# Performance work log

Measured on AMD Instinct MI355X. Metric: run time of the kernel, lower is better.

## Reference

```python
import jax, jax.numpy as jnp
import numpy as np
import math

B, C_IN, H, W_DIM, D_DIM = 2, 128, 24, 24, 24
D_MODEL, N_HEAD, N_LAYERS, D_FF = 256, 8, 4, 512
D_K = D_MODEL // N_HEAD
EPS = 1e-6


def setup_inputs() -> dict:
    key = jax.random.key(0)
    ks = jax.random.split(key, 16)
    s = 0.02
    inp = {
        "x": jax.random.normal(ks[0], (B, C_IN, H, W_DIM, D_DIM), jnp.float32),
        # 1x1x1 Conv3d W_x: weight [out, in], bias [out]
        "Wx_w": jax.random.normal(ks[1], (D_MODEL, C_IN), jnp.float32) * s,
        "Wx_b": jnp.zeros((D_MODEL,), jnp.float32),
        # per-layer attention projections (stacked over layers)
        "Wq": jax.random.normal(ks[2], (N_LAYERS, D_MODEL, D_MODEL), jnp.float32) * s,
        "bq": jnp.zeros((N_LAYERS, D_MODEL), jnp.float32),
        "Wk": jax.random.normal(ks[3], (N_LAYERS, D_MODEL, D_MODEL), jnp.float32) * s,
        "bk": jnp.zeros((N_LAYERS, D_MODEL), jnp.float32),
        "Wv": jax.random.normal(ks[4], (N_LAYERS, D_MODEL, D_MODEL), jnp.float32) * s,
        "bv": jnp.zeros((N_LAYERS, D_MODEL), jnp.float32),
        "Wo": jax.random.normal(ks[5], (N_LAYERS, D_MODEL, D_MODEL), jnp.float32) * s,
        "bo": jnp.zeros((N_LAYERS, D_MODEL), jnp.float32),
        # layer norms
        "ln1_g": jnp.ones((N_LAYERS, D_MODEL), jnp.float32),
        "ln1_b": jnp.zeros((N_LAYERS, D_MODEL), jnp.float32),
        "ln2_g": jnp.ones((N_LAYERS, D_MODEL), jnp.float32),
        "ln2_b": jnp.zeros((N_LAYERS, D_MODEL), jnp.float32),
        # FFN
        "ffn_w1": jax.random.normal(ks[6], (N_LAYERS, D_MODEL, D_FF), jnp.float32) * s,
        "ffn_b1": jnp.zeros((N_LAYERS, D_FF), jnp.float32),
        "ffn_w2": jax.random.normal(ks[7], (N_LAYERS, D_FF, D_MODEL), jnp.float32) * s,
        "ffn_b2": jnp.zeros((N_LAYERS, D_MODEL), jnp.float32),
        # depthwise 3x3x3 conv positional encoder (groups = D_MODEL)
        "pos_w": jax.random.normal(ks[8], (N_LAYERS, D_MODEL, 1, 3, 3, 3), jnp.float32) * s,
        "pos_b": jnp.zeros((N_LAYERS, D_MODEL), jnp.float32),
    }
    return inp


def _layer_norm(t, g, b):
    mu = jnp.mean(t, axis=-1, keepdims=True)
    var = jnp.var(t, axis=-1, keepdims=True)
    return (t - mu) * jax.lax.rsqrt(var + EPS) * g + b


def reference(x, Wx_w, Wx_b, Wq, bq, Wk, bk, Wv, bv, Wo, bo,
              ln1_g, ln1_b, ln2_g, ln2_b,
              ffn_w1, ffn_b1, ffn_w2, ffn_b2, pos_w, pos_b):
    b = x.shape[0]
    # 1x1x1 conv projection W_x + ReLU (is_up=False path)
    x = jnp.einsum('bchwd,oc->bohwd', x, Wx_w) + Wx_b[None, :, None, None, None]
    x = jax.nn.relu(x)

    inv_sqrt_dk = 1.0 / math.sqrt(D_K)

    for i in range(N_LAYERS):
        # flatten spatial -> tokens: [b, n, d_model]
        t = jnp.transpose(x.reshape(b, D_MODEL, -1), (0, 2, 1))
        n = t.shape[1]

        def heads(y):  # [b,n,d] -> [b,h,n,dk]
            return jnp.transpose(y.reshape(b, n, N_HEAD, D_K), (0, 2, 1, 3))

        q = heads(t @ Wq[i] + bq[i])
        k = heads(t @ Wk[i] + bk[i])
        v = heads(t @ Wv[i] + bv[i])

        # linear attention: softmax over feature dim for q, token dim for k
        q = jax.nn.softmax(q, axis=-1) * inv_sqrt_dk
        k = jax.nn.softmax(k, axis=-2)
        ctx = jnp.einsum('bhnd,bhne->bhde', k, v)     # [b,h,dk,dk]
        o = jnp.einsum('bhnd,bhde->bhne', q, ctx)      # [b,h,n,dk]
        o = jnp.transpose(o, (0, 2, 1, 3)).reshape(b, n, D_MODEL)
        o = o @ Wo[i] + bo[i]

        t = _layer_norm(t + o, ln1_g[i], ln1_b[i])
        f = jax.nn.gelu(t @ ffn_w1[i] + ffn_b1[i], approximate=False) @ ffn_w2[i] + ffn_b2[i]
        t = _layer_norm(t + f, ln2_g[i], ln2_b[i])

        # back to volume and depthwise conv positional embedding
        x = jnp.transpose(t, (0, 2, 1)).reshape(b, D_MODEL, H, W_DIM, D_DIM)
        pos = jax.lax.conv_general_dilated(
            x, pos_w[i], window_strides=(1, 1, 1), padding='SAME',
            dimension_numbers=('NCDHW', 'OIDHW', 'NCDHW'),
            feature_group_count=D_MODEL,
        ) + pos_b[i][None, :, None, None, None]
        x = x + pos
    return x
```

## Files before the change

kernel.cpp:

```cpp
#include <hip/hip_runtime.h>
#include <math.h>

#define NTOK 13824
#define MTOT 27648
#define BATCH 2
#define CIN 128
#define DMODEL 256
#define NHEAD 8
#define NLAYERS 4
#define DFF 512
#define NSPLIT 27
#define KVHALF ((size_t)BATCH * 256 * NTOK)

typedef float f32x4 __attribute__((ext_vector_type(4)));
typedef __bf16 bf16x8 __attribute__((ext_vector_type(8)));
typedef __attribute__((address_space(1))) void gvoid;
typedef __attribute__((address_space(3))) void lvoid;

#define GLDS16(g, l) __builtin_amdgcn_global_load_lds((gvoid*)(g), (lvoid*)(l), 16, 0, 0)

__device__ __forceinline__ unsigned short f2bf(float f) {
    unsigned u = __float_as_uint(f);
    return (unsigned short)((u + 0x7FFFu + ((u >> 16) & 1u)) >> 16);
}
__device__ __forceinline__ float bf2f(unsigned short h) {
    return __uint_as_float(((unsigned)h) << 16);
}

template<int ACT, int OUTM>
__global__ __launch_bounds__(256) void gemm_bf16(
    const unsigned short* __restrict__ A, int lda,
    const unsigned short* __restrict__ Bt, int ldb,
    const float* __restrict__ bias,
    float* __restrict__ Cf, unsigned short* __restrict__ Cb,
    int ldc, int K, long sA, long sB, long sC)
{
    A  += (size_t)blockIdx.z * sA;
    Bt += (size_t)blockIdx.z * sB;
    if (OUTM == 2) Cf += (size_t)blockIdx.z * sC;
    Cb += (size_t)blockIdx.z * sC;

    int bx, by;
    {
        const int nx  = gridDim.x;
        const int q   = (nx * gridDim.y) >> 3;
        const int lin = blockIdx.y * nx + blockIdx.x;
        const int wg  = (lin & 7) * q + (lin >> 3);
        bx = wg % nx;
        by = wg / nx;
    }

    __shared__ __attribute__((aligned(16))) unsigned short As[2][8192];
    __shared__ __attribute__((aligned(16))) unsigned short Bs[2][8192];
    const int t    = threadIdx.x;
    const int lane = t & 63;
    const int wave = t >> 6;
    const int wm = wave & 1, wn = wave >> 1;
    const int m0 = bx * 128, n0 = by * 128;

    const int srow = t >> 3;
    const int skid = ((t & 7) * 8) ^ ((srow & 7) << 3);
    const unsigned short* ga = A  + (size_t)(m0 + srow) * lda + skid;
    const unsigned short* gb = Bt + (size_t)(n0 + srow) * ldb + skid;

    f32x4 acc[4][4];
    #pragma unroll
    for (int i = 0; i < 4; ++i)
        #pragma unroll
        for (int j = 0; j < 4; ++j) acc[i][j] = (f32x4)0.0f;

    const int fm  = lane & 15;
    const int fq8 = (lane >> 4) * 8;
    const int sw3 = (fm & 7) << 3;
    const int arow = (wm * 64 + fm) * 64;
    const int brow = (wn * 64 + fm) * 64;

#define STAGE(bufi, kk)                                                        \
    {                                                                          \
        _Pragma("unroll")                                                      \
        for (int p = 0; p < 4; ++p) {                                          \
            GLDS16(ga + (size_t)p * 32 * lda + (kk), &As[bufi][p * 2048 + t * 8]); \
            GLDS16(gb + (size_t)p * 32 * ldb + (kk), &Bs[bufi][p * 2048 + t * 8]); \
        }                                                                      \
    }

#define COMPUTE(bufi)                                                          \
    {                                                                          \
        _Pragma("unroll")                                                      \
        for (int ks = 0; ks < 2; ++ks) {                                       \
            bf16x8 af[4], bg[4];                                               \
            const int kidx = (fq8 + ks * 32) ^ sw3;                            \
            _Pragma("unroll")                                                  \
            for (int i = 0; i < 4; ++i)                                        \
                af[i] = *(const bf16x8*)(&As[bufi][arow + i * 1024 + kidx]);   \
            _Pragma("unroll")                                                  \
            for (int j = 0; j < 4; ++j)                                        \
                bg[j] = *(const bf16x8*)(&Bs[bufi][brow + j * 1024 + kidx]);   \
            _Pragma("unroll")                                                  \
            for (int i = 0; i < 4; ++i)                                        \
                _Pragma("unroll")                                              \
                for (int j = 0; j < 4; ++j)                                    \
                    acc[i][j] = __builtin_amdgcn_mfma_f32_16x16x32_bf16(       \
                        af[i], bg[j], acc[i][j], 0, 0, 0);                     \
        }                                                                      \
    }

    STAGE(0, 0)
    __syncthreads();
    const int NT = K >> 6;
    int cur = 0;
    for (int t64 = 0; t64 < NT - 1; ++t64) {
        STAGE(cur ^ 1, (t64 + 1) * 64)
        COMPUTE(cur)
        __syncthreads();
        cur ^= 1;
    }
    COMPUTE(cur)

#undef STAGE
#undef COMPUTE

    if constexpr (ACT == 3) {
        const int cb  = n0 + wn * 64 + fm;
        const int rbs = m0 + wm * 64 + (lane >> 4) * 4;
        #pragma unroll
        for (int i = 0; i < 4; ++i) {
            #pragma unroll
            for (int r = 0; r < 4; ++r) {
                const int row = rbs + i * 16 + r;
                const float bv = bias[row];
                const size_t base = (row < 256)
                    ? (size_t)row * NTOK
                    : KVHALF + (size_t)(row - 256) * NTOK;
                #pragma unroll
                for (int j = 0; j < 4; ++j) {
                    float v = acc[i][j][r] + bv;
                    if (row < 256) v = __expf(v);
                    Cb[base + cb + j * 16] = f2bf(v);
                }
            }
        }
        return;
    }

    if constexpr (OUTM == 1) {
        __syncthreads();
        unsigned short* cs =
            (wave < 2 ? &As[0][0] : &Bs[0][0]) + (wave & 1) * 4608;
        const int rb4 = (lane >> 4) * 4;
        #pragma unroll
        for (int j = 0; j < 4; ++j) {
            const float bv = bias[n0 + wn * 64 + j * 16 + fm];
            #pragma unroll
            for (int i = 0; i < 4; ++i)
                #pragma unroll
                for (int r = 0; r < 4; ++r) {
                    float v = acc[i][j][r] + bv;
                    if (ACT == 1) v = fmaxf(v, 0.0f);
                    if (ACT == 2) v = 0.5f * v * (1.0f + erff(v * 0.7071067811865476f));
                    cs[(i * 16 + rb4 + r) * 72 + j * 16 + fm] = f2bf(v);
                }
        }
        const size_t gb = (size_t)(m0 + wm * 64) * ldc + n0 + wn * 64;
        const int rl = lane >> 3, sg = (lane & 7) * 8;
        #pragma unroll
        for (int it = 0; it < 8; ++it) {
            const int row = it * 8 + rl;
            const uint4 val = *(const uint4*)(cs + row * 72 + sg);
            *(uint4*)(Cb + gb + (size_t)row * ldc + sg) = val;
        }
        return;
    }

    const int cb  = n0 + wn * 64 + fm;
    const int rbs = m0 + wm * 64 + (lane >> 4) * 4;
    #pragma unroll
    for (int j = 0; j < 4; ++j) {
        const int n = cb + j * 16;
        const float bv = bias[n];
        #pragma unroll
        for (int i = 0; i < 4; ++i) {
            #pragma unroll
            for (int r = 0; r < 4; ++r) {
                float v = acc[i][j][r] + bv;
                if (ACT == 1) v = fmaxf(v, 0.0f);
                if (ACT == 2) v = 0.5f * v * (1.0f + erff(v * 0.7071067811865476f));
                const size_t off = (size_t)(rbs + i * 16 + r) * ldc + n;
                if (OUTM == 2) Cf[off] = v;
                Cb[off] = f2bf(v);
            }
        }
    }
}

#define CW_QKV  786432
#define CW_O   1048576
#define CW_1   1572864
#define CW_2   2097152
#define CW_X   2129920
#define CW_B   2132992
__global__ __launch_bounds__(256) void conv_weights(
    const float* __restrict__ Wq, const float* __restrict__ Wk,
    const float* __restrict__ Wv, const float* __restrict__ Wo,
    const float* __restrict__ fw1, const float* __restrict__ fw2,
    const float* __restrict__ Wx_w,
    const float* __restrict__ bq, const float* __restrict__ bk,
    const float* __restrict__ bv,
    unsigned short* __restrict__ wqkv_t, unsigned short* __restrict__ wo_t,
    unsigned short* __restrict__ w1_t, unsigned short* __restrict__ w2_t,
    unsigned short* __restrict__ wx_bf, float* __restrict__ bqkv)
{
    const int e = blockIdx.x * 256 + threadIdx.x;
    if (e < CW_QKV) {
        const int i = e / 196608, r = e % 196608;
        const int n = r / 256, k = r % 256;
        const float* src = (n < 256) ? Wq : (n < 512) ? Wk : Wv;
        wqkv_t[e] = f2bf(src[((size_t)i * 256 + k) * 256 + (n & 255)]);
    } else if (e < CW_O) {
        const int r = e - CW_QKV;
        const int i = r / 65536, rr = r % 65536, n = rr / 256, k = rr % 256;
        wo_t[r] = f2bf(Wo[((size_t)i * 256 + k) * 256 + n]);
    } else if (e < CW_1) {
        const int r = e - CW_O;
        const int i = r / 131072, rr = r % 131072, n = rr / 256, k = rr % 256;
        w1_t[r] = f2bf(fw1[((size_t)i * 256 + k) * 512 + n]);
    } else if (e < CW_2) {
        const int r = e - CW_1;
        const int i = r / 131072, rr = r % 131072, n = rr / 512, k = rr % 512;
        w2_t[r] = f2bf(fw2[((size_t)i * 512 + k) * 256 + n]);
    } else if (e < CW_X) {
        const int r = e - CW_2;
        wx_bf[r] = f2bf(Wx_w[r]);
    } else if (e < CW_B) {
        const int r = e - CW_X;
        const int i = r / 768, j = r % 768;
        const float v = (j < 256) ? bq[i * 256 + j]
                      : (j < 512) ? bk[i * 256 + j - 256]
                                  : bv[i * 256 + j - 512];
        bqkv[r] = v;
    }
}

__global__ __launch_bounds__(256) void conv_x(
    const float* __restrict__ x, unsigned short* __restrict__ xbf)
{
    __shared__ float tile[32][33];
    const int n0 = blockIdx.x * 32;
    const int c0 = blockIdx.y * 32;
    const int b  = blockIdx.z;
    const int t = threadIdx.x;
    const int tn = t & 31, tc = t >> 5;
    #pragma unroll
    for (int p = 0; p < 4; ++p)
        tile[tc + p * 8][tn] =
            x[((size_t)(b * CIN + c0 + tc + p * 8)) * NTOK + n0 + tn];
    __syncthreads();
    const int cc = t & 31, nr = t >> 5;
    #pragma unroll
    for (int p = 0; p < 4; ++p)
        xbf[((size_t)(b * NTOK + n0 + nr + p * 8)) * CIN + c0 + cc] =
            f2bf(tile[cc][nr + p * 8]);
}

__global__ __launch_bounds__(256) void qsm_kernel(unsigned short* __restrict__ qbuf)
{
    const int g = blockIdx.x * 256 + threadIdx.x;
    const int row = g >> 5;
    const int cg  = g & 31;
    unsigned short* p = qbuf + (size_t)row * 256 + cg * 8;
    uint4 raw = *(const uint4*)p;
    unsigned short* rp = (unsigned short*)&raw;
    float v[8];
    #pragma unroll
    for (int j = 0; j < 8; ++j) v[j] = bf2f(rp[j]);
    float m = v[0];
    #pragma unroll
    for (int j = 1; j < 8; ++j) m = fmaxf(m, v[j]);
    m = fmaxf(m, __shfl_xor(m, 1, 64));
    m = fmaxf(m, __shfl_xor(m, 2, 64));
    float s = 0.0f;
    #pragma unroll
    for (int j = 0; j < 8; ++j) { v[j] = __expf(v[j] - m); s += v[j]; }
    s += __shfl_xor(s, 1, 64);
    s += __shfl_xor(s, 2, 64);
    const float r = 1.0f / s;
    #pragma unroll
    for (int j = 0; j < 8; ++j) rp[j] = f2bf(v[j] * r);
    *(uint4*)p = raw;
}

__global__ __launch_bounds__(256) void ctx_mfma(
    const unsigned short* __restrict__ kvT,
    float* __restrict__ ctxp, float* __restrict__ skp)
{
    const int s = blockIdx.x, h = blockIdx.y, b = blockIdx.z;
    const int t = threadIdx.x, w = t >> 6, l = t & 63;
    const int fm = l & 15, fq = (l >> 4) * 8;
    const size_t rowA = (size_t)(b * 256 + h * 32 + fm) * NTOK;
    const int n0 = s * 512 + w * 128 + fq;
    const unsigned short* pa = kvT + rowA + n0;
    const unsigned short* pb = kvT + KVHALF + rowA + n0;

    f32x4 acc[2][2];
    #pragma unroll
    for (int x = 0; x < 2; ++x)
        #pragma unroll
        for (int y = 0; y < 2; ++y) acc[x][y] = (f32x4)0.0f;
    float ss0 = 0.0f, ss1 = 0.0f;

    #pragma unroll
    for (int step = 0; step < 4; ++step) {
        const int ko = step * 32;
        const uint4 ra0 = *(const uint4*)(pa + ko);
        const uint4 ra1 = *(const uint4*)(pa + (size_t)16 * NTOK + ko);
        const uint4 rb0 = *(const uint4*)(pb + ko);
        const uint4 rb1 = *(const uint4*)(pb + (size_t)16 * NTOK + ko);
        const bf16x8 a0 = *(const bf16x8*)&ra0;
        const bf16x8 a1 = *(const bf16x8*)&ra1;
        const bf16x8 b0 = *(const bf16x8*)&rb0;
        const bf16x8 b1 = *(const bf16x8*)&rb1;
        acc[0][0] = __builtin_amdgcn_mfma_f32_16x16x32_bf16(a0, b0, acc[0][0], 0, 0, 0);
        acc[0][1] = __builtin_amdgcn_mfma_f32_16x16x32_bf16(a0, b1, acc[0][1], 0, 0, 0);
        acc[1][0] = __builtin_amdgcn_mfma_f32_16x16x32_bf16(a1, b0, acc[1][0], 0, 0, 0);
        acc[1][1] = __builtin_amdgcn_mfma_f32_16x16x32_bf16(a1, b1, acc[1][1], 0, 0, 0);
        const unsigned short* u0 = (const unsigned short*)&ra0;
        const unsigned short* u1 = (const unsigned short*)&ra1;
        #pragma unroll
        for (int j = 0; j < 8; ++j) { ss0 += bf2f(u0[j]); ss1 += bf2f(u1[j]); }
    }

    ss0 += __shfl_xor(ss0, 16, 64); ss0 += __shfl_xor(ss0, 32, 64);
    ss1 += __shfl_xor(ss1, 16, 64); ss1 += __shfl_xor(ss1, 32, 64);
    __shared__ float skw[4][32];
    __shared__ float redc[4][32][33];
    if (l < 16) { skw[w][fm] = ss0; skw[w][16 + fm] = ss1; }

    const int rb4 = (l >> 4) * 4;
    #pragma unroll
    for (int x = 0; x < 2; ++x)
        #pragma unroll
        for (int y = 0; y < 2; ++y)
            #pragma unroll
            for (int r = 0; r < 4; ++r)
                redc[w][x * 16 + rb4 + r][y * 16 + fm] = acc[x][y][r];
    __syncthreads();

    if (t < 32)
        skp[(size_t)s * 512 + b * 256 + h * 32 + t] =
            skw[0][t] + skw[1][t] + skw[2][t] + skw[3][t];

    const int e0 = t * 4;
    const int dd = e0 >> 5, c0 = e0 & 31;
    float4 o;
    o.x = redc[0][dd][c0+0] + redc[1][dd][c0+0] + redc[2][dd][c0+0] + redc[3][dd][c0+0];
    o.y = redc[0][dd][c0+1] + redc[1][dd][c0+1] + redc[2][dd][c0+1] + redc[3][dd][c0+1];
    o.z = redc[0][dd][c0+2] + redc[1][dd][c0+2] + redc[2][dd][c0+2] + redc[3][dd][c0+2];
    o.w = redc[0][dd][c0+3] + redc[1][dd][c0+3] + redc[2][dd][c0+3] + redc[3][dd][c0+3];
    *(float4*)(ctxp + ((size_t)s * 16 + b * 8 + h) * 1024 + e0) = o;
}

__global__ __launch_bounds__(256) void ctxred(
    const float* __restrict__ ctxp, const float* __restrict__ skp,
    float* __restrict__ ctx, float* __restrict__ Sk)
{
    const int o = blockIdx.x * 256 + threadIdx.x;
    if (o < 16384) {
        float a = 0.0f;
        for (int s = 0; s < NSPLIT; ++s) a += ctxp[(size_t)s * 16384 + o];
        ctx[o] = a;
    } else {
        const int c = o - 16384;
        float a = 0.0f;
        for (int s = 0; s < NSPLIT; ++s) a += skp[(size_t)s * 512 + c];
        Sk[c] = a;
    }
}

__global__ __launch_bounds__(256) void ctxwo_kernel(
    const float* __restrict__ ctx, const float* __restrict__ Sk,
    const unsigned short* __restrict__ wo_t, unsigned short* __restrict__ wp)
{
    const int h = blockIdx.x, b = blockIdx.y;
    const int n = threadIdx.x;
    __shared__ float cl[1024];
    __shared__ float sdk[32];
    {
        const float* cp = ctx + (size_t)(b * 8 + h) * 1024;
        *(float4*)&cl[n * 4] = *(const float4*)&cp[n * 4];
    }
    if (n < 32) sdk[n] = 0.17677669529663687f / Sk[b * 256 + h * 32 + n];
    __syncthreads();
    float w[32];
    const unsigned short* wop = wo_t + (size_t)n * 256 + h * 32;
    #pragma unroll
    for (int e = 0; e < 32; ++e) w[e] = bf2f(wop[e]);
    unsigned short outv[32];
    #pragma unroll
    for (int d = 0; d < 32; ++d) {
        float acc = 0.0f;
        #pragma unroll
        for (int e = 0; e < 32; ++e) acc += cl[d * 32 + e] * w[e];
        outv[d] = f2bf(acc * sdk[d]);
    }
    unsigned short* op = wp + (size_t)b * 65536 + (size_t)n * 256 + h * 32;
    #pragma unroll
    for (int d = 0; d < 32; d += 8)
        *(uint4*)(op + d) = *(uint4*)(outv + d);
}

template<int WB>
__global__ __launch_bounds__(256) void ln8_kernel(
    float* __restrict__ t, const unsigned short* __restrict__ add,
    const float* __restrict__ g, const float* __restrict__ bta,
    unsigned short* __restrict__ tbf)
{
    const int l  = threadIdx.x & 31;
    const int rg = threadIdx.x >> 5;
    const size_t row = (size_t)blockIdx.x * 8 + rg;
    const size_t off = row * 256 + l * 8;

    const float4 a0 = *(const float4*)(t + off);
    const float4 a1 = *(const float4*)(t + off + 4);
    const uint4  ad = *(const uint4*)(add + off);
    const unsigned short* ap = (const unsigned short*)&ad;

    float v[8] = {a0.x, a0.y, a0.z, a0.w, a1.x, a1.y, a1.z, a1.w};
    float s = 0.0f;
    #pragma unroll
    for (int k = 0; k < 8; ++k) { v[k] += bf2f(ap[k]); s += v[k]; }
    #pragma unroll
    for (int o = 16; o; o >>= 1) s += __shfl_xor(s, o, 32);
    const float mu = s * (1.0f / 256.0f);

    float s2 = 0.0f;
    #pragma unroll
    for (int k = 0; k < 8; ++k) { v[k] -= mu; s2 += v[k] * v[k]; }
    #pragma unroll
    for (int o = 16; o; o >>= 1) s2 += __shfl_xor(s2, o, 32);
    const float rs = rsqrtf(s2 * (1.0f / 256.0f) + 1e-6f);

    const float4 g0 = *(const float4*)(g + l * 8);
    const float4 g1 = *(const float4*)(g + l * 8 + 4);
    const float4 b0 = *(const float4*)(bta + l * 8);
    const float4 b1 = *(const float4*)(bta + l * 8 + 4);
    const float gg[8] = {g0.x, g0.y, g0.z, g0.w, g1.x, g1.y, g1.z, g1.w};
    const float bb[8] = {b0.x, b0.y, b0.z, b0.w, b1.x, b1.y, b1.z, b1.w};

    float o8[8];
    #pragma unroll
    for (int k = 0; k < 8; ++k) o8[k] = v[k] * rs * gg[k] + bb[k];

    *(float4*)(t + off)     = make_float4(o8[0], o8[1], o8[2], o8[3]);
    *(float4*)(t + off + 4) = make_float4(o8[4], o8[5], o8[6], o8[7]);
    if (WB) {
        uint4 ob_;
        unsigned short* op = (unsigned short*)&ob_;
        #pragma unroll
        for (int k = 0; k < 8; ++k) op[k] = f2bf(o8[k]);
        *(uint4*)(tbf + off) = ob_;
    }
}

#define DSEG 8
template<int WB>
__global__ __launch_bounds__(256) void posconv_kernel(
    const float* __restrict__ tin, const float* __restrict__ pw,
    const float* __restrict__ pb, float* __restrict__ outp,
    unsigned short* __restrict__ tbfp)
{
    const int hw  = blockIdx.x;
    const int d0  = blockIdx.y * DSEG;
    const int b   = blockIdx.z;
    const int hh = hw / 24, ww = hw % 24;
    const int c  = threadIdx.x;

    float w[27];
    #pragma unroll
    for (int k = 0; k < 27; ++k) w[k] = pw[c * 27 + k];
    const float bias = pb[c];

    const float* base = tin + (size_t)b * NTOK * 256 + c;

    const float* colp[9];
    bool colok[9];
    #pragma unroll
    for (int dh = -1; dh <= 1; ++dh)
        #pragma unroll
        for (int dw = -1; dw <= 1; ++dw) {
            const int j = (dh + 1) * 3 + (dw + 1);
            const int h2 = hh + dh, w2 = ww + dw;
            colok[j] = ((unsigned)h2 < 24u) & ((unsigned)w2 < 24u);
            colp[j] = base + (size_t)((h2 * 24 + w2) * 24 + d0) * 256;
        }

    float win[9][3];
    #pragma unroll
    for (int j = 0; j < 9; ++j) {
        win[j][0] = (colok[j] && d0 > 0) ? colp[j][-256] : 0.0f;
        win[j][1] = colok[j] ? colp[j][0] : 0.0f;
    }

    if constexpr (WB == 2) {
        float oseg[DSEG];
        #pragma unroll
        for (int dd = 0; dd < DSEG; ++dd) {
            #pragma unroll
            for (int j = 0; j < 9; ++j)
                win[j][2] = (colok[j] && (d0 + dd < 23)) ? colp[j][(dd + 1) * 256] : 0.0f;
            float acc = bias + win[4][1];
            #pragma unroll
            for (int j = 0; j < 9; ++j) {
                acc += w[j * 3 + 0] * win[j][0];
                acc += w[j * 3 + 1] * win[j][1];
                acc += w[j * 3 + 2] * win[j][2];
            }
            oseg[dd] = acc;
            #pragma unroll
            for (int j = 0; j < 9; ++j) { win[j][0] = win[j][1]; win[j][1] = win[j][2]; }
        }
        float* op = outp + ((size_t)b * 256 + c) * NTOK + hw * 24 + d0;
        #pragma unroll
        for (int q = 0; q < DSEG / 4; ++q)
            *(float4*)(op + q * 4) =
                make_float4(oseg[q*4], oseg[q*4+1], oseg[q*4+2], oseg[q*4+3]);
        return;
    }

    float* ob = outp + ((size_t)b * NTOK + (size_t)hw * 24 + d0) * 256 + c;
    unsigned short* tb = (WB == 1)
        ? (tbfp + ((size_t)b * NTOK + (size_t)hw * 24 + d0) * 256 + c)
        : (unsigned short*)nullptr;

    #pragma unroll
    for (int dd = 0; dd < DSEG; ++dd) {
        #pragma unroll
        for (int j = 0; j < 9; ++j)
            win[j][2] = (colok[j] && (d0 + dd < 23)) ? colp[j][(dd + 1) * 256] : 0.0f;

        float acc = bias + win[4][1];
        #pragma unroll
        for (int j = 0; j < 9; ++j) {
            acc += w[j * 3 + 0] * win[j][0];
            acc += w[j * 3 + 1] * win[j][1];
            acc += w[j * 3 + 2] * win[j][2];
        }
        ob[dd * 256] = acc;
        if (WB == 1) tb[dd * 256] = f2bf(acc);

        #pragma unroll
        for (int j = 0; j < 9; ++j) { win[j][0] = win[j][1]; win[j][1] = win[j][2]; }
    }
}

extern "C" void kernel_launch(void* const* d_in, const int* in_sizes, int n_in,
                              void* d_out, int out_size, void* d_ws, size_t ws_size,
                              hipStream_t stream)
{
    (void)in_sizes; (void)n_in; (void)out_size; (void)ws_size;
    const float* x     = (const float*)d_in[0];
    const float* Wx_w  = (const float*)d_in[1];
    const float* Wx_b  = (const float*)d_in[2];
    const float* Wq    = (const float*)d_in[3];
    const float* bq    = (const float*)d_in[4];
    const float* Wk    = (const float*)d_in[5];
    const float* bk    = (const float*)d_in[6];
    const float* Wv    = (const float*)d_in[7];
    const float* bv    = (const float*)d_in[8];
    const float* Wo    = (const float*)d_in[9];
    const float* bo    = (const float*)d_in[10];
    const float* ln1_g = (const float*)d_in[11];
    const float* ln1_b = (const float*)d_in[12];
    const float* ln2_g = (const float*)d_in[13];
    const float* ln2_b = (const float*)d_in[14];
    const float* fw1   = (const float*)d_in[15];
    const float* fb1   = (const float*)d_in[16];
    const float* fw2   = (const float*)d_in[17];
    const float* fb2   = (const float*)d_in[18];
    const float* pw    = (const float*)d_in[19];
    const float* pb    = (const float*)d_in[20];
    float* out = (float*)d_out;

    char* p = (char*)d_ws;
    float* tA            = (float*)p;          p += (size_t)MTOT * 256 * 4;
    float* tB            = (float*)p;          p += (size_t)MTOT * 256 * 4;
    unsigned short* tbf  = (unsigned short*)p; p += (size_t)MTOT * 256 * 2;
    unsigned short* qbuf = (unsigned short*)p; p += (size_t)MTOT * 256 * 2;
    unsigned short* hbf  = (unsigned short*)p; p += (size_t)MTOT * 512 * 2;
    unsigned short* ob   = (unsigned short*)p; p += (size_t)MTOT * 256 * 2;
    unsigned short* xbf  = (unsigned short*)p; p += (size_t)MTOT * 128 * 2;
    unsigned short* wqkv_t = (unsigned short*)p; p += (size_t)786432 * 2;
    unsigned short* wo_t   = (unsigned short*)p; p += (size_t)262144 * 2;
    unsigned short* w1_t   = (unsigned short*)p; p += (size_t)524288 * 2;
    unsigned short* w2_t   = (unsigned short*)p; p += (size_t)524288 * 2;
    unsigned short* wx_bf  = (unsigned short*)p; p += (size_t)32768 * 2;
    unsigned short* wp     = (unsigned short*)p; p += (size_t)BATCH * 65536 * 2;
    float* bqkv = (float*)p; p += 3072 * 4;
    float* ctx  = (float*)p; p += 16384 * 4;
    float* Sk   = (float*)p; p += 512 * 4;
    float* ctxp = (float*)p; p += (size_t)NSPLIT * 16384 * 4;
    float* skp  = (float*)p; p += (size_t)NSPLIT * 512 * 4;
    unsigned short* kvT = hbf;

    hipLaunchKernelGGL(conv_weights, dim3(8333), dim3(256), 0, stream,
                       Wq, Wk, Wv, Wo, fw1, fw2, Wx_w, bq, bk, bv,
                       wqkv_t, wo_t, w1_t, w2_t, wx_bf, bqkv);
    hipLaunchKernelGGL(conv_x, dim3(NTOK / 32, CIN / 32, BATCH), dim3(256), 0, stream,
                       x, xbf);

    hipLaunchKernelGGL((gemm_bf16<1, 2>), dim3(216, 2, 1), dim3(256), 0, stream,
                       xbf, CIN, wx_bf, CIN, Wx_b, tA, tbf, 256, CIN,
                       (long)0, (long)0, (long)0);

    for (int i = 0; i < NLAYERS; ++i) {
        float* tin  = (i & 1) ? tB : tA;
        float* tout = (i & 1) ? tA : tB;

        hipLaunchKernelGGL((gemm_bf16<0, 1>), dim3(216, 2, 1), dim3(256), 0, stream,
                           tbf, 256, wqkv_t + (size_t)i * 196608, 256,
                           bqkv + i * 768, nullptr, qbuf, 256, 256,
                           (long)0, (long)0, (long)0);

        hipLaunchKernelGGL((gemm_bf16<3, 1>), dim3(4, 108, BATCH), dim3(256), 0, stream,
                           wqkv_t + (size_t)i * 196608 + 65536, 256,
                           tbf, 256, bqkv + i * 768 + 256,
                           nullptr, kvT, 0, 256,
                           (long)0, (long)NTOK * 256, (long)256 * NTOK);

        hipLaunchKernelGGL(ctx_mfma, dim3(NSPLIT, NHEAD, BATCH), dim3(256), 0, stream,
                           kvT, ctxp, skp);
        hipLaunchKernelGGL(ctxred, dim3(66), dim3(256), 0, stream, ctxp, skp, ctx, Sk);

        hipLaunchKernelGGL(qsm_kernel, dim3(3456), dim3(256), 0, stream, qbuf);
        hipLaunchKernelGGL(ctxwo_kernel, dim3(NHEAD, BATCH), dim3(256), 0, stream,
                           ctx, Sk, wo_t + (size_t)i * 65536, wp);

        hipLaunchKernelGGL((gemm_bf16<0, 1>), dim3(108, 2, BATCH), dim3(256), 0, stream,
                           qbuf, 256, wp, 256, bo + i * 256, nullptr, ob, 256, 256,
                           (long)NTOK * 256, (long)65536, (long)NTOK * 256);

        hipLaunchKernelGGL((ln8_kernel<1>), dim3(MTOT / 8), dim3(256), 0, stream,
                           tin, ob, ln1_g + i * 256, ln1_b + i * 256, tbf);

        hipLaunchKernelGGL((gemm_bf16<2, 1>), dim3(216, 4, 1), dim3(256), 0, stream,
                           tbf, 256, w1_t + (size_t)i * 131072, 256,
                           fb1 + i * 512, nullptr, hbf, 512, 256,
                           (long)0, (long)0, (long)0);
        hipLaunchKernelGGL((gemm_bf16<0, 1>), dim3(216, 2, 1), dim3(256), 0, stream,
                           hbf, 512, w2_t + (size_t)i * 131072, 512,
                           fb2 + i * 256, nullptr, ob, 256, 512,
                           (long)0, (long)0, (long)0);
        hipLaunchKernelGGL((ln8_kernel<0>), dim3(MTOT / 8), dim3(256), 0, stream,
                           tin, ob, ln2_g + i * 256, ln2_b + i * 256, nullptr);

        if (i < NLAYERS - 1)
            hipLaunchKernelGGL((posconv_kernel<1>), dim3(576, 3, BATCH), dim3(256), 0, stream,
                               tin, pw + (size_t)i * 6912, pb + i * 256, tout, tbf);
        else
            hipLaunchKernelGGL((posconv_kernel<2>), dim3(576, 3, BATCH), dim3(256), 0, stream,
                               tin, pw + (size_t)i * 6912, pb + i * 256, out, nullptr);
    }
}
```

Baseline: 791.8 us.

## Add register-resident weight GEMM for K=256 projections, replacing LDS-tiled GEMM

Adds a gemm_pb kernel for K=256 GEMMs. Each wave holds a 64-column slice of the weight matrix in registers for the whole K, then streams 16-row A fragments straight from global memory with no LDS staging or barriers. It replaces the LDS-tiled GEMM for the Q projection, the attention output projection and the first FFN layer, and removes the old LDS-staged coalesced store path. The cost is heavy register use (128 VGPRs just for the B fragments), uncoalesced 2-byte scattered output stores, and A tiles reloaded from global memory once per column block.

```diff
diff --git a/kernel.cpp b/kernel.cpp
--- a/kernel.cpp
+++ b/kernel.cpp
@@ -25,6 +25,75 @@
 }
 __device__ __forceinline__ float bf2f(unsigned short h) {
     return __uint_as_float(((unsigned)h) << 16);
+}
+
+template<int ACT, int G>
+__global__ __launch_bounds__(256) void gemm_pb(
+    const unsigned short* __restrict__ A,
+    const unsigned short* __restrict__ Bt,
+    const float* __restrict__ bias,
+    unsigned short* __restrict__ Cb, int ldc,
+    long sA, long sB, long sC)
+{
+    A  += (size_t)blockIdx.z * sA;
+    Bt += (size_t)blockIdx.z * sB;
+    Cb += (size_t)blockIdx.z * sC;
+
+    int bx = blockIdx.x;
+    { const int nx = gridDim.x; bx = (bx & 7) * (nx >> 3) + (bx >> 3); }
+
+    const int lane = threadIdx.x & 63;
+    const int wave = threadIdx.x >> 6;
+    const int fm   = lane & 15;
+    const int fq8  = (lane >> 4) * 8;
+    const int colbase = blockIdx.y * 256 + wave * 64;
+
+    bf16x8 bg[4][8];
+    {
+        const unsigned short* bp = Bt + (size_t)(colbase + fm) * 256 + fq8;
+        #pragma unroll
+        for (int j = 0; j < 4; ++j)
+            #pragma unroll
+            for (int ks = 0; ks < 8; ++ks)
+                bg[j][ks] = *(const bf16x8*)(bp + (size_t)j * 16 * 256 + ks * 32);
+    }
+
+    const float bv0 = bias[colbase + fm];
+    const float bv1 = bias[colbase + 16 + fm];
+    const float bv2 = bias[colbase + 32 + fm];
+    const float bv3 = bias[colbase + 48 + fm];
+
+    const int row0 = bx * (G * 16);
+    for (int g = 0; g < G; ++g) {
+        const int mr = row0 + g * 16;
+        const unsigned short* ap = A + (size_t)(mr + fm) * 256 + fq8;
+        bf16x8 af[8];
+        #pragma unroll
+        for (int ks = 0; ks < 8; ++ks)
+            af[ks] = *(const bf16x8*)(ap + ks * 32);
+
+        f32x4 acc[4];
+        #pragma unroll
+        for (int j = 0; j < 4; ++j) acc[j] = (f32x4)0.0f;
+        #pragma unroll
+        for (int ks = 0; ks < 8; ++ks)
+            #pragma unroll
+            for (int j = 0; j < 4; ++j)
+                acc[j] = __builtin_amdgcn_mfma_f32_16x16x32_bf16(
+                    af[ks], bg[j][ks], acc[j], 0, 0, 0);
+
+        const int rb = mr + (lane >> 4) * 4;
+        #pragma unroll
+        for (int j = 0; j < 4; ++j) {
+            const float bvj = (j == 0) ? bv0 : (j == 1) ? bv1 : (j == 2) ? bv2 : bv3;
+            #pragma unroll
+            for (int r = 0; r < 4; ++r) {
+                float v = acc[j][r] + bvj;
+                if (ACT == 2) v = 0.5f * v * (1.0f + erff(v * 0.7071067811865476f));
+                Cb[(size_t)(rb + r) * ldc + colbase + j * 16 + fm] = f2bf(v);
+            }
+        }
+    }
 }
 
 template<int ACT, int OUTM>
@@ -139,35 +208,6 @@
                     Cb[base + cb + j * 16] = f2bf(v);
                 }
             }
-        }
-        return;
-    }
-
-    if constexpr (OUTM == 1) {
-        __syncthreads();
-        unsigned short* cs =
-            (wave < 2 ? &As[0][0] : &Bs[0][0]) + (wave & 1) * 4608;
-        const int rb4 = (lane >> 4) * 4;
-        #pragma unroll
-        for (int j = 0; j < 4; ++j) {
-            const float bv = bias[n0 + wn * 64 + j * 16 + fm];
-            #pragma unroll
-            for (int i = 0; i < 4; ++i)
-                #pragma unroll
-                for (int r = 0; r < 4; ++r) {
-                    float v = acc[i][j][r] + bv;
-                    if (ACT == 1) v = fmaxf(v, 0.0f);
-                    if (ACT == 2) v = 0.5f * v * (1.0f + erff(v * 0.7071067811865476f));
-                    cs[(i * 16 + rb4 + r) * 72 + j * 16 + fm] = f2bf(v);
-                }
-        }
-        const size_t gb = (size_t)(m0 + wm * 64) * ldc + n0 + wn * 64;
-        const int rl = lane >> 3, sg = (lane & 7) * 8;
-        #pragma unroll
-        for (int it = 0; it < 8; ++it) {
-            const int row = it * 8 + rl;
-            const uint4 val = *(const uint4*)(cs + row * 72 + sg);
-            *(uint4*)(Cb + gb + (size_t)row * ldc + sg) = val;
         }
         return;
     }
@@ -615,9 +655,9 @@
         float* tin  = (i & 1) ? tB : tA;
         float* tout = (i & 1) ? tA : tB;
 
-        hipLaunchKernelGGL((gemm_bf16<0, 1>), dim3(216, 2, 1), dim3(256), 0, stream,
-                           tbf, 256, wqkv_t + (size_t)i * 196608, 256,
-                           bqkv + i * 768, nullptr, qbuf, 256, 256,
+        hipLaunchKernelGGL((gemm_pb<0, 4>), dim3(432, 1, 1), dim3(256), 0, stream,
+                           tbf, wqkv_t + (size_t)i * 196608,
+                           bqkv + i * 768, qbuf, 256,
                            (long)0, (long)0, (long)0);
 
         hipLaunchKernelGGL((gemm_bf16<3, 1>), dim3(4, 108, BATCH), dim3(256), 0, stream,
@@ -634,16 +674,16 @@
         hipLaunchKernelGGL(ctxwo_kernel, dim3(NHEAD, BATCH), dim3(256), 0, stream,
                            ctx, Sk, wo_t + (size_t)i * 65536, wp);
 
-        hipLaunchKernelGGL((gemm_bf16<0, 1>), dim3(108, 2, BATCH), dim3(256), 0, stream,
-                           qbuf, 256, wp, 256, bo + i * 256, nullptr, ob, 256, 256,
+        hipLaunchKernelGGL((gemm_pb<0, 4>), dim3(216, 1, BATCH), dim3(256), 0, stream,
+                           qbuf, wp, bo + i * 256, ob, 256,
                            (long)NTOK * 256, (long)65536, (long)NTOK * 256);
 
         hipLaunchKernelGGL((ln8_kernel<1>), dim3(MTOT / 8), dim3(256), 0, stream,
                            tin, ob, ln1_g + i * 256, ln1_b + i * 256, tbf);
 
-        hipLaunchKernelGGL((gemm_bf16<2, 1>), dim3(216, 4, 1), dim3(256), 0, stream,
-                           tbf, 256, w1_t + (size_t)i * 131072, 256,
-                           fb1 + i * 512, nullptr, hbf, 512, 256,
+        hipLaunchKernelGGL((gemm_pb<2, 4>), dim3(432, 2, 1), dim3(256), 0, stream,
+                           tbf, w1_t + (size_t)i * 131072,
+                           fb1 + i * 512, hbf, 512,
                            (long)0, (long)0, (long)0);
         hipLaunchKernelGGL((gemm_bf16<0, 1>), dim3(216, 2, 1), dim3(256), 0, stream,
                            hbf, 512, w2_t + (size_t)i * 131072, 512,
```

New measurement: 917.4 us. +15.9%, slower.
